# Kernel optimization log

Measured on AMD Instinct MI355X. Metric: run time of the kernel, lower is better.

The kernel has to match this reference:

```python
import jax, jax.numpy as jnp
import numpy as np

N_NODES = 100000
N_EDGES = 1200000
NODE_DIM = 128
HIDDEN = 64
N_POSTS = 50000


def setup_inputs() -> dict:
    key = jax.random.key(0)
    ks = jax.random.split(key, 10)
    s = 1.0 / np.sqrt(NODE_DIM)
    sh = 1.0 / np.sqrt(HIDDEN)
    return {
        "node_features": jax.random.normal(ks[0], (N_NODES, NODE_DIM), dtype=jnp.float32),
        "edge_index": jax.random.randint(ks[1], (2, N_EDGES), 0, N_NODES, dtype=jnp.int64) if jax.config.jax_enable_x64 else jax.random.randint(ks[1], (2, N_EDGES), 0, N_NODES, dtype=jnp.int32),
        "post_mask": jax.random.randint(ks[2], (N_POSTS,), 0, N_NODES, dtype=jnp.int32),
        "W_enc": jax.random.uniform(ks[3], (NODE_DIM, HIDDEN), jnp.float32, -s, s),
        "b_enc": jax.random.uniform(ks[4], (HIDDEN,), jnp.float32, -s, s),
        "W_conv": jax.random.uniform(ks[5], (HIDDEN, HIDDEN), jnp.float32, -sh, sh),
        "b_conv": jax.random.uniform(ks[6], (HIDDEN,), jnp.float32, -sh, sh),
        "W_out": jax.random.uniform(ks[7], (HIDDEN, 1), jnp.float32, -sh, sh),
        "b_out": jax.random.uniform(ks[8], (1,), jnp.float32, -sh, sh),
    }


def reference(node_features, edge_index, post_mask, W_enc, b_enc, W_conv, b_conv, W_out, b_out):
    # encode: relu(Linear)
    node_emb = jax.nn.relu(node_features @ W_enc + b_enc)  # [N, H]
    src, dst = edge_index[0], edge_index[1]
    # per-edge gather then scatter-add into destination nodes (segment sum)
    messages = jax.ops.segment_sum(node_emb[src], dst, num_segments=node_emb.shape[0])  # [N, H]
    node_emb = jax.nn.relu((node_emb + messages) @ W_conv + b_conv)  # [N, H]
    post_emb = node_emb[post_mask]  # [P, H]
    out = jax.nn.sigmoid((post_emb @ W_out + b_out).squeeze(-1))  # [P]
    return out
```

## Files before the change

### kernel.cpp

```cpp
#include <hip/hip_runtime.h>
#include <hip/hip_bf16.h>
#include <math.h>


#define HIDDEN 64
#define NODE_DIM 128
#define SCAN_CHUNK 1024

typedef __attribute__((ext_vector_type(8))) short short8;
typedef __attribute__((ext_vector_type(4))) float floatx4;

union F2B { short8 s; __hip_bfloat162 h[4]; };

__device__ inline short8 cvt8(const float4& p, const float4& q) {
    F2B u;
    u.h[0] = __float22bfloat162_rn(make_float2(p.x, p.y));
    u.h[1] = __float22bfloat162_rn(make_float2(p.z, p.w));
    u.h[2] = __float22bfloat162_rn(make_float2(q.x, q.y));
    u.h[3] = __float22bfloat162_rn(make_float2(q.z, q.w));
    return u.s;
}

__device__ inline void cvt8_split(const float4& p, const float4& q,
                                  short8& hi, short8& lo) {
    const float f[8] = {p.x, p.y, p.z, p.w, q.x, q.y, q.z, q.w};
    F2B uh, ul;
    #pragma unroll
    for (int jj = 0; jj < 4; ++jj) {
        const float2 v = make_float2(f[2 * jj], f[2 * jj + 1]);
        const __hip_bfloat162 h = __float22bfloat162_rn(v);
        const float2 hv = __bfloat1622float2(h);
        ul.h[jj] = __float22bfloat162_rn(make_float2(v.x - hv.x, v.y - hv.y));
        uh.h[jj] = h;
    }
    hi = uh.s; lo = ul.s;
}

__global__ __launch_bounds__(256) void k_setflags(
    const int* __restrict__ post, unsigned int* __restrict__ bits,
    int* __restrict__ nodelist, int* __restrict__ listCnt, int n_posts)
{
    const int p = blockIdx.x * 256 + threadIdx.x;
    if (p >= n_posts) return;
    const int n = post[p];
    const unsigned int bit = 1u << (n & 31);
    const unsigned int old = atomicOr(&bits[n >> 5], bit);
    if (!(old & bit)) {
        const int i = atomicAdd(listCnt, 1);
        nodelist[i] = n;
    }
}

__global__ __launch_bounds__(256) void k_encode_mfma(
    const float* __restrict__ A, const float* __restrict__ We,
    const float* __restrict__ be, __hip_bfloat16* __restrict__ emb16,
    int* __restrict__ count, int n_nodes, int n_tiles)
{
    const int gtid = blockIdx.x * 256 + threadIdx.x;
    if (gtid < n_nodes) count[gtid] = 0;

    const int lane = threadIdx.x & 63;
    const int r    = lane & 15;
    const int quad = lane >> 4;

    short8 Wb[4][4];
    #pragma unroll
    for (int ks = 0; ks < 4; ++ks)
        #pragma unroll
        for (int nt = 0; nt < 4; ++nt) {
            F2B u;
            #pragma unroll
            for (int jj = 0; jj < 4; ++jj) {
                const int k0 = ks * 32 + quad * 8 + 2 * jj;
                const float lo = We[(size_t)k0 * HIDDEN + nt * 16 + r];
                const float hi = We[(size_t)(k0 + 1) * HIDDEN + nt * 16 + r];
                u.h[jj] = __float22bfloat162_rn(make_float2(lo, hi));
            }
            Wb[ks][nt] = u.s;
        }
    float bias[4];
    #pragma unroll
    for (int nt = 0; nt < 4; ++nt) bias[nt] = be[nt * 16 + r];

    const int wid    = (blockIdx.x * 256 + threadIdx.x) >> 6;
    const int nwaves = gridDim.x * 4;
    for (int t = wid; t < n_tiles; t += nwaves) {
        const float* Arow = A + (size_t)t * 16 * NODE_DIM + (size_t)r * NODE_DIM + quad * 8;
        float4 a[4][2];
        #pragma unroll
        for (int ks = 0; ks < 4; ++ks) {
            a[ks][0] = *(const float4*)(Arow + ks * 32);
            a[ks][1] = *(const float4*)(Arow + ks * 32 + 4);
        }
        floatx4 acc[4] = {};
        #pragma unroll
        for (int ks = 0; ks < 4; ++ks) {
            const short8 af = cvt8(a[ks][0], a[ks][1]);
            #pragma unroll
            for (int nt = 0; nt < 4; ++nt)
                acc[nt] = __builtin_amdgcn_mfma_f32_16x16x32_bf16(af, Wb[ks][nt], acc[nt], 0, 0, 0);
        }
        #pragma unroll
        for (int nt = 0; nt < 4; ++nt)
            #pragma unroll
            for (int g = 0; g < 4; ++g) {
                const int node = t * 16 + quad * 4 + g;
                const float h = fmaxf(acc[nt][g] + bias[nt], 0.0f);
                emb16[(size_t)node * HIDDEN + nt * 16 + r] = __float2bfloat16(h);
            }
    }
    const int rem = n_nodes - n_tiles * 16;
    if (rem > 0 && wid == 0) {
        for (int n = n_tiles * 16; n < n_nodes; ++n) {
            float acc = be[lane];
            const float* row = A + (size_t)n * NODE_DIM;
            for (int k = 0; k < NODE_DIM; ++k)
                acc = fmaf(row[k], We[(size_t)k * HIDDEN + lane], acc);
            emb16[(size_t)n * HIDDEN + lane] = __float2bfloat16(fmaxf(acc, 0.0f));
        }
    }
}

__global__ __launch_bounds__(256) void k_count(
    const int* __restrict__ dsts, const unsigned int* __restrict__ bits,
    int* __restrict__ count, int n_edges)
{
    const int stride = gridDim.x * 256;
    for (int e = blockIdx.x * 256 + threadIdx.x; e < n_edges; e += stride) {
        const int d = dsts[e];
        if ((bits[d >> 5] >> (d & 31)) & 1u) atomicAdd(&count[d], 1);
    }
}

__global__ __launch_bounds__(256) void k_scan_lb(
    const int* __restrict__ count, int* __restrict__ row_start,
    unsigned int* __restrict__ partials, int n)
{
    __shared__ int s[256];
    __shared__ int sExc;
    const int b = blockIdx.x, tid = threadIdx.x;
    const int base = b * SCAN_CHUNK + tid * 4;
    int c0 = (base + 0 < n) ? count[base + 0] : 0;
    int c1 = (base + 1 < n) ? count[base + 1] : 0;
    int c2 = (base + 2 < n) ? count[base + 2] : 0;
    int c3 = (base + 3 < n) ? count[base + 3] : 0;
    const int t = c0 + c1 + c2 + c3;
    s[tid] = t;
    __syncthreads();
    #pragma unroll
    for (int off = 1; off < 256; off <<= 1) {
        int v = (tid >= off) ? s[tid - off] : 0;
        __syncthreads();
        s[tid] += v;
        __syncthreads();
    }
    if (tid == 0) {
        const unsigned int total = (unsigned int)s[255];
        if (b == 0) {
            __hip_atomic_store(&partials[0], (2u << 30) | total,
                               __ATOMIC_RELEASE, __HIP_MEMORY_SCOPE_AGENT);
            sExc = 0;
        } else {
            __hip_atomic_store(&partials[b], (1u << 30) | total,
                               __ATOMIC_RELEASE, __HIP_MEMORY_SCOPE_AGENT);
            int exc = 0, j = b - 1;
            while (true) {
                const unsigned int v = __hip_atomic_load(&partials[j],
                    __ATOMIC_ACQUIRE, __HIP_MEMORY_SCOPE_AGENT);
                const unsigned int st = v >> 30;
                if (st == 0u) { __builtin_amdgcn_s_sleep(1); continue; }
                exc += (int)(v & 0x3FFFFFFFu);
                if (st == 2u) break;
                --j;
            }
            __hip_atomic_store(&partials[b], (2u << 30) | (unsigned int)(exc + (int)total),
                               __ATOMIC_RELEASE, __HIP_MEMORY_SCOPE_AGENT);
            sExc = exc;
        }
    }
    __syncthreads();
    int run = sExc + s[tid] - t;
    if (base + 0 < n) row_start[base + 0] = run;           run += c0;
    if (base + 1 < n) row_start[base + 1] = run;           run += c1;
    if (base + 2 < n) row_start[base + 2] = run;           run += c2;
    if (base + 3 < n) row_start[base + 3] = run;
}

__global__ __launch_bounds__(256) void k_fill(
    const int* __restrict__ srcs, const int* __restrict__ dsts,
    const unsigned int* __restrict__ bits, int* __restrict__ row_start,
    int* __restrict__ slots, int n_edges)
{
    const int stride = gridDim.x * 256;
    for (int e = blockIdx.x * 256 + threadIdx.x; e < n_edges; e += stride) {
        const int d = dsts[e];
        if (!((bits[d >> 5] >> (d & 31)) & 1u)) continue;
        const int idx = atomicAdd(&row_start[d], 1);
        slots[idx] = srcs[e];
    }
}

__global__ __launch_bounds__(256) void k_gather(
    const int* __restrict__ nodelist, const int* __restrict__ listCnt,
    const int* __restrict__ row_end, const int* __restrict__ count,
    const int* __restrict__ slots, const __hip_bfloat16* __restrict__ emb16,
    float* __restrict__ msg_c)
{
    const int lane = threadIdx.x & 63;
    const int j    = lane & 7;
    const int g    = lane >> 3;
    const int gw   = (blockIdx.x * 256 + threadIdx.x) >> 6;
    const int nw   = gridDim.x * 4;
    const int nc   = listCnt[0];

    for (int i = gw; i < nc; i += nw) {
        const int n    = nodelist[i];
        const int m    = count[n];
        const int base = row_end[n] - m;

        float2 a0 = {0.f, 0.f}, a1 = {0.f, 0.f}, a2 = {0.f, 0.f}, a3 = {0.f, 0.f};
        #define ACC8(v)  do { F2B u; u.s = (v); float2 t;                       \
            t = __bfloat1622float2(u.h[0]); a0.x += t.x; a0.y += t.y;           \
            t = __bfloat1622float2(u.h[1]); a1.x += t.x; a1.y += t.y;           \
            t = __bfloat1622float2(u.h[2]); a2.x += t.x; a2.y += t.y;           \
            t = __bfloat1622float2(u.h[3]); a3.x += t.x; a3.y += t.y; } while (0)

        if (g == 0) {
            const short8 v = *(const short8*)(emb16 + (size_t)n * HIDDEN + j * 8);
            ACC8(v);
        }
        int c = g;
        for (; c + 8 < m; c += 16) {
            const int s0 = slots[base + c];
            const int s1 = slots[base + c + 8];
            const short8 v0 = *(const short8*)(emb16 + (size_t)s0 * HIDDEN + j * 8);
            const short8 v1 = *(const short8*)(emb16 + (size_t)s1 * HIDDEN + j * 8);
            ACC8(v0); ACC8(v1);
        }
        for (; c < m; c += 8) {
            const int s0 = slots[base + c];
            const short8 v0 = *(const short8*)(emb16 + (size_t)s0 * HIDDEN + j * 8);
            ACC8(v0);
        }
        #undef ACC8

        #pragma unroll
        for (int off = 8; off < 64; off <<= 1) {
            a0.x += __shfl_xor(a0.x, off); a0.y += __shfl_xor(a0.y, off);
            a1.x += __shfl_xor(a1.x, off); a1.y += __shfl_xor(a1.y, off);
            a2.x += __shfl_xor(a2.x, off); a2.y += __shfl_xor(a2.y, off);
            a3.x += __shfl_xor(a3.x, off); a3.y += __shfl_xor(a3.y, off);
        }
        if (g == 0) {
            float4* dst = (float4*)(msg_c + (size_t)i * HIDDEN + j * 8);
            dst[0] = make_float4(a0.x, a0.y, a1.x, a1.y);
            dst[1] = make_float4(a2.x, a2.y, a3.x, a3.y);
        }
    }
}

__global__ __launch_bounds__(256) void k_head_mfma(
    const int* __restrict__ listCnt, const int* __restrict__ nodelist,
    const float* __restrict__ msg_c,
    const float* __restrict__ Wc, const float* __restrict__ bc,
    const float* __restrict__ Wo, const float* __restrict__ bo,
    float* __restrict__ res)
{
    const int lane = threadIdx.x & 63;
    const int r    = lane & 15;
    const int quad = lane >> 4;

    short8 Wb[2][4];
    #pragma unroll
    for (int ks = 0; ks < 2; ++ks)
        #pragma unroll
        for (int nt = 0; nt < 4; ++nt) {
            F2B u;
            #pragma unroll
            for (int jj = 0; jj < 4; ++jj) {
                const int k0 = ks * 32 + quad * 8 + 2 * jj;
                const float lo = Wc[(size_t)k0 * HIDDEN + nt * 16 + r];
                const float hi = Wc[(size_t)(k0 + 1) * HIDDEN + nt * 16 + r];
                u.h[jj] = __float22bfloat162_rn(make_float2(lo, hi));
            }
            Wb[ks][nt] = u.s;
        }
    float bias[4], wo[4];
    #pragma unroll
    for (int nt = 0; nt < 4; ++nt) { bias[nt] = bc[nt * 16 + r]; wo[nt] = Wo[nt * 16 + r]; }
    const float bo_s = bo[0];

    const int nc      = listCnt[0];
    const int n_tiles = (nc + 15) / 16;
    const int wid     = (blockIdx.x * 256 + threadIdx.x) >> 6;
    const int nwaves  = gridDim.x * 4;

    for (int tile = wid; tile < n_tiles; tile += nwaves) {
        const int i0  = tile * 16;
        const int row = i0 + r;
        floatx4 acc[4] = {};
        #pragma unroll
        for (int ks = 0; ks < 2; ++ks) {
            float4 f0 = make_float4(0.f, 0.f, 0.f, 0.f), f1 = f0;
            if (row < nc) {
                const float* src = msg_c + (size_t)row * HIDDEN + ks * 32 + quad * 8;
                f0 = *(const float4*)src;
                f1 = *(const float4*)(src + 4);
            }
            short8 ah, al;
            cvt8_split(f0, f1, ah, al);
            #pragma unroll
            for (int nt = 0; nt < 4; ++nt) {
                acc[nt] = __builtin_amdgcn_mfma_f32_16x16x32_bf16(ah, Wb[ks][nt], acc[nt], 0, 0, 0);
                acc[nt] = __builtin_amdgcn_mfma_f32_16x16x32_bf16(al, Wb[ks][nt], acc[nt], 0, 0, 0);
            }
        }
        float r4[4];
        #pragma unroll
        for (int gg = 0; gg < 4; ++gg) {
            float part = 0.0f;
            #pragma unroll
            for (int nt = 0; nt < 4; ++nt)
                part += fmaxf(acc[nt][gg] + bias[nt], 0.0f) * wo[nt];
            part += __shfl_xor(part, 1);
            part += __shfl_xor(part, 2);
            part += __shfl_xor(part, 4);
            part += __shfl_xor(part, 8);
            r4[gg] = part;
        }
        if (r == 0) {
            #pragma unroll
            for (int gg = 0; gg < 4; ++gg) {
                const int idx = i0 + quad * 4 + gg;
                if (idx < nc)
                    res[nodelist[idx]] = 1.0f / (1.0f + __expf(-(r4[gg] + bo_s)));
            }
        }
    }
}

__global__ __launch_bounds__(256) void k_out(
    const int* __restrict__ post, const float* __restrict__ res,
    float* __restrict__ out, int n_posts)
{
    const int p = blockIdx.x * 256 + threadIdx.x;
    if (p < n_posts) out[p] = res[post[p]];
}

extern "C" void kernel_launch(void* const* d_in, const int* in_sizes, int n_in,
                              void* d_out, int out_size, void* d_ws, size_t ws_size,
                              hipStream_t stream) {
    const float* A    = (const float*)d_in[0];
    const int*   ei   = (const int*)  d_in[1];
    const int*   post = (const int*)  d_in[2];
    const float* We   = (const float*)d_in[3];
    const float* be   = (const float*)d_in[4];
    const float* Wc   = (const float*)d_in[5];
    const float* bc   = (const float*)d_in[6];
    const float* Wo   = (const float*)d_in[7];
    const float* bo   = (const float*)d_in[8];
    float* out = (float*)d_out;

    const int n_nodes = in_sizes[0] / NODE_DIM;
    const int n_edges = in_sizes[1] / 2;
    const int n_posts = in_sizes[2];

    char* p = (char*)d_ws;
    __hip_bfloat16* emb16 = (__hip_bfloat16*)p;  p += (size_t)n_nodes * HIDDEN * 2;
    float* msg_c    = (float*)p;              p += (size_t)n_posts * HIDDEN * 4;
    int*   slots    = (int*)p;                p += (size_t)n_edges * 4;
    char* zbase = p;
    unsigned int* bits = (unsigned int*)p;    p += ((size_t)(n_nodes + 31) / 32 + 32) * 4;
    int*   listCnt  = (int*)p;                p += 256;
    unsigned int* partials = (unsigned int*)p; p += 1024;
    const size_t zbytes = (size_t)(p - zbase);
    int*   count    = (int*)p;                p += (size_t)n_nodes * 4;
    int*   row_start= (int*)p;                p += (size_t)n_nodes * 4;
    int*   nodelist = (int*)p;                p += (size_t)n_nodes * 4;
    float* res      = (float*)p;              p += (size_t)n_nodes * 4;

    const int* srcs = ei;
    const int* dsts = ei + n_edges;
    const int nb = (n_nodes + SCAN_CHUNK - 1) / SCAN_CHUNK;
    const int n_tiles = n_nodes / 16;

    hipMemsetAsync(zbase, 0, zbytes, stream);
    k_setflags<<<(n_posts + 255) / 256, 256, 0, stream>>>(post, bits, nodelist, listCnt, n_posts);
    k_encode_mfma<<<(n_tiles + 3) / 4, 256, 0, stream>>>(A, We, be, emb16, count, n_nodes, n_tiles);
    k_count<<<2048, 256, 0, stream>>>(dsts, bits, count, n_edges);
    k_scan_lb<<<nb, 256, 0, stream>>>(count, row_start, partials, n_nodes);
    k_fill<<<2048, 256, 0, stream>>>(srcs, dsts, bits, row_start, slots, n_edges);
    k_gather<<<8192, 256, 0, stream>>>(nodelist, listCnt, row_start, count, slots, emb16, msg_c);
    k_head_mfma<<<1024, 256, 0, stream>>>(listCnt, nodelist, msg_c, Wc, bc, Wo, bo, res);
    k_out<<<(n_posts + 255) / 256, 256, 0, stream>>>(post, res, out, n_posts);
}
```

Measured before the change: 220.6 us.

## Fuse count-zeroing into flag kernel, edge counting into encode, parallelize scan lookback

Moves zeroing of the per-node count array into the post-flag kernel and appends the edge-count loop to the encode kernel, removing one launch. The single-thread decoupled lookback in the scan becomes a 64-lane windowed lookback that uses ballots and a shuffle reduction. The aim is less launch overhead and shorter serial lookback chains. The count loop now runs with the encode grid size instead of a fixed 2048 blocks, and the fused kernel may use more registers.

```diff
diff --git a/kernel.cpp b/kernel.cpp
--- a/kernel.cpp
+++ b/kernel.cpp
@@ -36,29 +36,30 @@
     hi = uh.s; lo = ul.s;
 }
 
-__global__ __launch_bounds__(256) void k_setflags(
+__global__ __launch_bounds__(256) void k_pre(
     const int* __restrict__ post, unsigned int* __restrict__ bits,
-    int* __restrict__ nodelist, int* __restrict__ listCnt, int n_posts)
-{
-    const int p = blockIdx.x * 256 + threadIdx.x;
-    if (p >= n_posts) return;
-    const int n = post[p];
-    const unsigned int bit = 1u << (n & 31);
-    const unsigned int old = atomicOr(&bits[n >> 5], bit);
-    if (!(old & bit)) {
-        const int i = atomicAdd(listCnt, 1);
-        nodelist[i] = n;
-    }
-}
-
-__global__ __launch_bounds__(256) void k_encode_mfma(
+    int* __restrict__ nodelist, int* __restrict__ listCnt,
+    int* __restrict__ count, int n_posts, int n_nodes)
+{
+    const int gtid = blockIdx.x * 256 + threadIdx.x;
+    if (gtid < n_nodes) count[gtid] = 0;
+    if (gtid < n_posts) {
+        const int n = post[gtid];
+        const unsigned int bit = 1u << (n & 31);
+        const unsigned int old = atomicOr(&bits[n >> 5], bit);
+        if (!(old & bit)) {
+            const int i = atomicAdd(listCnt, 1);
+            nodelist[i] = n;
+        }
+    }
+}
+
+__global__ __launch_bounds__(256) void k_encode_count(
     const float* __restrict__ A, const float* __restrict__ We,
     const float* __restrict__ be, __hip_bfloat16* __restrict__ emb16,
-    int* __restrict__ count, int n_nodes, int n_tiles)
-{
-    const int gtid = blockIdx.x * 256 + threadIdx.x;
-    if (gtid < n_nodes) count[gtid] = 0;
-
+    const int* __restrict__ dsts, const unsigned int* __restrict__ bits,
+    int* __restrict__ count, int n_nodes, int n_tiles, int n_edges)
+{
     const int lane = threadIdx.x & 63;
     const int r    = lane & 15;
     const int quad = lane >> 4;
@@ -119,12 +120,7 @@
             emb16[(size_t)n * HIDDEN + lane] = __float2bfloat16(fmaxf(acc, 0.0f));
         }
     }
-}
-
-__global__ __launch_bounds__(256) void k_count(
-    const int* __restrict__ dsts, const unsigned int* __restrict__ bits,
-    int* __restrict__ count, int n_edges)
-{
+
     const int stride = gridDim.x * 256;
     for (int e = blockIdx.x * 256 + threadIdx.x; e < n_edges; e += stride) {
         const int d = dsts[e];
@@ -154,28 +150,57 @@
         s[tid] += v;
         __syncthreads();
     }
-    if (tid == 0) {
-        const unsigned int total = (unsigned int)s[255];
-        if (b == 0) {
-            __hip_atomic_store(&partials[0], (2u << 30) | total,
+    const int total = s[255];
+
+    if (b == 0) {
+        if (tid == 0) {
+            __hip_atomic_store(&partials[0], (2u << 30) | (unsigned int)total,
                                __ATOMIC_RELEASE, __HIP_MEMORY_SCOPE_AGENT);
             sExc = 0;
-        } else {
-            __hip_atomic_store(&partials[b], (1u << 30) | total,
+        }
+    } else {
+        if (tid == 0) {
+            __hip_atomic_store(&partials[b], (1u << 30) | (unsigned int)total,
                                __ATOMIC_RELEASE, __HIP_MEMORY_SCOPE_AGENT);
-            int exc = 0, j = b - 1;
+        }
+        if (tid < 64) {
+            int exc = 0;
+            int winEnd = b;
             while (true) {
-                const unsigned int v = __hip_atomic_load(&partials[j],
-                    __ATOMIC_ACQUIRE, __HIP_MEMORY_SCOPE_AGENT);
+                const int j = winEnd - 64 + tid;
+                const unsigned int v = (j >= 0)
+                    ? __hip_atomic_load(&partials[j], __ATOMIC_ACQUIRE,
+                                        __HIP_MEMORY_SCOPE_AGENT)
+                    : (2u << 30);
                 const unsigned int st = v >> 30;
-                if (st == 0u) { __builtin_amdgcn_s_sleep(1); continue; }
-                exc += (int)(v & 0x3FFFFFFFu);
-                if (st == 2u) break;
-                --j;
-            }
-            __hip_atomic_store(&partials[b], (2u << 30) | (unsigned int)(exc + (int)total),
-                               __ATOMIC_RELEASE, __HIP_MEMORY_SCOPE_AGENT);
-            sExc = exc;
+                if (__ballot(st == 0u)) {
+                    __builtin_amdgcn_s_sleep(1);
+                    continue;
+                }
+                const unsigned long long b2 = __ballot(st == 2u);
+                int contrib;
+                bool done;
+                if (b2) {
+                    const int hi = 63 - __clzll(b2);
+                    contrib = (tid >= hi) ? (int)(v & 0x3FFFFFFFu) : 0;
+                    done = true;
+                } else {
+                    contrib = (int)(v & 0x3FFFFFFFu);
+                    done = false;
+                }
+                #pragma unroll
+                for (int off = 1; off < 64; off <<= 1)
+                    contrib += __shfl_xor(contrib, off);
+                exc += contrib;
+                if (done) break;
+                winEnd -= 64;
+            }
+            if (tid == 0) {
+                __hip_atomic_store(&partials[b],
+                                   (2u << 30) | (unsigned int)(exc + total),
+                                   __ATOMIC_RELEASE, __HIP_MEMORY_SCOPE_AGENT);
+                sExc = exc;
+            }
         }
     }
     __syncthreads();
@@ -385,9 +410,8 @@
     const int n_tiles = n_nodes / 16;
 
     hipMemsetAsync(zbase, 0, zbytes, stream);
-    k_setflags<<<(n_posts + 255) / 256, 256, 0, stream>>>(post, bits, nodelist, listCnt, n_posts);
-    k_encode_mfma<<<(n_tiles + 3) / 4, 256, 0, stream>>>(A, We, be, emb16, count, n_nodes, n_tiles);
-    k_count<<<2048, 256, 0, stream>>>(dsts, bits, count, n_edges);
+    k_pre<<<(n_nodes + 255) / 256, 256, 0, stream>>>(post, bits, nodelist, listCnt, count, n_posts, n_nodes);
+    k_encode_count<<<(n_tiles + 3) / 4, 256, 0, stream>>>(A, We, be, emb16, dsts, bits, count, n_nodes, n_tiles, n_edges);
     k_scan_lb<<<nb, 256, 0, stream>>>(count, row_start, partials, n_nodes);
     k_fill<<<2048, 256, 0, stream>>>(srcs, dsts, bits, row_start, slots, n_edges);
     k_gather<<<8192, 256, 0, stream>>>(nodelist, listCnt, row_start, count, slots, emb16, msg_c);
```

Measured after the change: 202.5 us. 1.09x faster.
